# Performance work log

Hardware: AMD Instinct MI355X
Metric: run time of the kernel (lower is better)

The kernel has to match this reference:

```python
import jax, jax.numpy as jnp
import numpy as np

B, V, W, H = 512, 256, 64, 64  # batch, num_variables, window, hidden_size


def setup_inputs() -> dict:
    key = jax.random.key(0)
    ks = jax.random.split(key, 10)
    s = 0.05
    return {
        "x": jax.random.normal(ks[0], (B, V, W), dtype=jnp.float32),
        # nn.LSTM(input=V, hidden=H): gate order i, f, g, o
        "w_ih": jax.random.normal(ks[1], (4 * H, V), dtype=jnp.float32) * s,
        "w_hh": jax.random.normal(ks[2], (4 * H, H), dtype=jnp.float32) * s,
        "b_ih": jax.random.normal(ks[3], (4 * H,), dtype=jnp.float32) * s,
        "b_hh": jax.random.normal(ks[4], (4 * H,), dtype=jnp.float32) * s,
        # linear_v: Linear(window, 1, bias=False)
        "w_v": jax.random.normal(ks[5], (1, W), dtype=jnp.float32) * s,
        # linear_w: Linear(2H, window)
        "w_w": jax.random.normal(ks[6], (W, 2 * H), dtype=jnp.float32) * s,
        "b_w": jax.random.normal(ks[7], (W,), dtype=jnp.float32) * s,
        # linear_u: Linear(window, window)
        "w_u": jax.random.normal(ks[8], (W, W), dtype=jnp.float32) * s,
        "b_u": jax.random.normal(ks[9], (W,), dtype=jnp.float32) * s,
    }


def reference(x, w_ih, w_hh, b_ih, b_hh, w_v, w_w, b_w, w_u, b_u):
    batch, n_var, window = x.shape
    hidden = w_hh.shape[1]
    # linear_u over the window (last) dim: (B, V, W)
    u_out = jnp.einsum("bvw,uw->bvu", x, w_u) + b_u
    x_steps = jnp.transpose(x, (2, 0, 1))  # (W, B, V)

    def step(carry, x_t):
        h, c = carry  # each (B, H)
        # input attention
        wout = jnp.concatenate([h, c], axis=1) @ w_w.T + b_w          # (B, W)
        score = jnp.einsum("bvw,w->bv", jnp.tanh(wout[:, None, :] + u_out), w_v[0])
        alpha = jax.nn.softmax(score, axis=1)                          # (B, V)
        x_tilde = alpha * x_t                                          # (B, V)
        # LSTM cell (torch gate order i, f, g, o)
        gates = x_tilde @ w_ih.T + b_ih + h @ w_hh.T + b_hh            # (B, 4H)
        i_g, f_g, g_g, o_g = jnp.split(gates, 4, axis=1)
        i_g = jax.nn.sigmoid(i_g)
        f_g = jax.nn.sigmoid(f_g)
        g_g = jnp.tanh(g_g)
        o_g = jax.nn.sigmoid(o_g)
        c_new = f_g * c + i_g * g_g
        h_new = o_g * jnp.tanh(c_new)
        return (h_new, c_new), (x_tilde, h_new)

    init = (jnp.zeros((batch, hidden), x.dtype), jnp.zeros((batch, hidden), x.dtype))
    _, (x_tilde_seq, h_seq) = jax.lax.scan(step, init, x_steps)
    # matches torch.stack(x_tilde_list) (W,B,V) and torch.stack(h_list) (W,B,H)
    return x_tilde_seq, h_seq
```

## Files before the change

### kernel.cpp

```cpp
#include <hip/hip_runtime.h>


#define KLOG2E  1.4426950408889634f
#define K2LOG2E 2.8853900817779268f

typedef _Float16 h2    __attribute__((ext_vector_type(2)));
typedef __fp16   f16x8 __attribute__((ext_vector_type(8)));
typedef float    f32x4 __attribute__((ext_vector_type(4)));
union H2U { h2 h; unsigned u; };

__device__ __forceinline__ float frcp(float x)  { return __builtin_amdgcn_rcpf(x); }
__device__ __forceinline__ float fexp2(float x) { return __builtin_amdgcn_exp2f(x); }
__device__ __forceinline__ float fsigmoid(float x) { return frcp(1.f + fexp2(-KLOG2E * x)); }
__device__ __forceinline__ float ftanh(float x) { return 1.f - 2.f * frcp(fexp2(K2LOG2E * x) + 1.f); }

__device__ __forceinline__ unsigned pkrtz_u(float a, float b) {
    H2U r; r.h = __builtin_bit_cast(h2, __builtin_amdgcn_cvt_pkrtz(a, b)); return r.u;
}
__device__ __forceinline__ h2 pk_rtn(float a, float b) {
    h2 r; r.x = (_Float16)a; r.y = (_Float16)b; return r;
}
__device__ __forceinline__ unsigned pk_rtn_u(float a, float b) {
    H2U r; r.h = pk_rtn(a, b); return r.u;
}

#define L_EHA  0
#define L_EHB  9216
#define L_WF   18432
#define L_PSA  34816
#define L_PSB  35072
#define L_XHA  35328
#define L_XHB  35456
#define L_EWA  35584
#define L_EWB  35648
#define L_HCA  35712
#define L_HCB  35840
#define L_HHA  35968
#define L_HHB  36000
#define L_BI   36032
#define L_WV   36288
#define L_WS   36352
#define L_TOT  36368

__global__ __launch_bounds__(1024, 4) void enc_kernel(
    const float* __restrict__ x,
    const float* __restrict__ w_ih,
    const float* __restrict__ w_hh,
    const float* __restrict__ b_ih,
    const float* __restrict__ b_hh,
    const float* __restrict__ w_v,
    const float* __restrict__ w_w,
    const float* __restrict__ b_w,
    const float* __restrict__ w_u,
    const float* __restrict__ b_u,
    float* __restrict__ out_xt,
    float* __restrict__ out_h)
{
    extern __shared__ float lds[];
    unsigned* EHA  = (unsigned*)(lds + L_EHA);
    unsigned* EHB  = (unsigned*)(lds + L_EHB);
    uint4*    WF4  = (uint4*)(lds + L_WF);
    float*    psA  = lds + L_PSA;   float* psB = lds + L_PSB;
    unsigned* xhA  = (unsigned*)(lds + L_XHA);
    unsigned* xhB  = (unsigned*)(lds + L_XHB);
    float*    ewA  = lds + L_EWA;   float* ewB = lds + L_EWB;
    float*    hcA  = lds + L_HCA;   float* hcB = lds + L_HCB;
    unsigned* hhA  = (unsigned*)(lds + L_HHA);
    unsigned* hhB  = (unsigned*)(lds + L_HHB);
    float*    biasL= lds + L_BI;
    float*    wv2L = lds + L_WV;
    float*    wsum = lds + L_WS;

    const int tid  = threadIdx.x;
    const int lane = tid & 63;
    const int wvi  = tid >> 6;
    const int bA   = blockIdx.x;
    const int bB   = blockIdx.x + 256;

    const int colw = wvi*16 + (lane & 15);
    const int kofs = (lane >> 4) * 8;

    const int w8 = wvi*4 + (lane >> 4);
    const int kg = lane & 15;
    const float4 www4 = *(const float4*)&w_w[w8*128 + kg*4];
    const float bwr = b_w[w8];
    float Sv = 0.f;
#pragma unroll
    for (int wi = 0; wi < 64; ++wi) Sv += w_v[wi];
    const float bu_lane = b_u[lane];

    if (tid < 256) biasL[tid] = b_ih[tid] + b_hh[tid];
    if (tid < 64)  wv2L[tid] = -2.f * w_v[tid];
    if (tid < 128) { hcA[tid] = 0.f; hcB[tid] = 0.f; }
    if (tid < 32)  { hhA[tid] = 0u; hhB[tid] = 0u; }

#pragma unroll 1
    for (int bb = 0; bb < 2; ++bb) {
        unsigned* EH = bb ? EHB : EHA;
        const int b = bb ? bB : bA;
        float a0[16];
        {
            float4 wu_r[8];
#pragma unroll
            for (int i = 0; i < 8; ++i) wu_r[i] = *(const float4*)&w_u[lane*64 + 4*i];
            const float* xb = x + b*16384;
#pragma unroll 2
            for (int vi = 0; vi < 16; ++vi) {
                int v = __builtin_amdgcn_readfirstlane(wvi*16 + vi);
                const float4* xr = (const float4*)(xb + v*64);
                float acc = 0.f;
#pragma unroll
                for (int i = 0; i < 8; ++i) {
                    float4 xx = xr[i]; float4 wu = wu_r[i];
                    acc += xx.x*wu.x + xx.y*wu.y + xx.z*wu.z + xx.w*wu.w;
                }
                a0[vi] = acc;
            }
        }
        {
            float4 wu_r[8];
#pragma unroll
            for (int i = 0; i < 8; ++i) wu_r[i] = *(const float4*)&w_u[lane*64 + 32 + 4*i];
            const float* xb = x + b*16384 + 32;
#pragma unroll 2
            for (int vi = 0; vi < 16; ++vi) {
                int v = __builtin_amdgcn_readfirstlane(wvi*16 + vi);
                const float4* xr = (const float4*)(xb + v*64);
                float acc = a0[vi] + bu_lane;
#pragma unroll
                for (int i = 0; i < 8; ++i) {
                    float4 xx = xr[i]; float4 wu = wu_r[i];
                    acc += xx.x*wu.x + xx.y*wu.y + xx.z*wu.z + xx.w*wu.w;
                }
                float e = fexp2(K2LOG2E * acc);
                float e2 = __shfl_xor(e, 1, 64);
                if (!(lane & 1)) EH[v*36 + (lane >> 1)] = pk_rtn_u(e, e2);
            }
        }
    }

    f16x8 wbx[4], wbh[2];
#pragma unroll
    for (int kk = 0; kk < 4; ++kk) {
        const float* s = w_ih + colw*256 + kk*32 + kofs;
        f16x8 a;
#pragma unroll
        for (int i = 0; i < 8; ++i) a[i] = (__fp16)s[i];
        wbx[kk] = a;
    }
#pragma unroll
    for (int kk = 0; kk < 2; ++kk) {
        const float* s = w_hh + colw*64 + kk*32 + kofs;
        f16x8 a;
#pragma unroll
        for (int i = 0; i < 8; ++i) a[i] = (__fp16)s[i];
        wbh[kk] = a;
    }
#pragma unroll
    for (int kk = 4; kk < 8; ++kk) {
        const float* s = w_ih + colw*256 + kk*32 + kofs;
        uint4 u;
        u.x = pk_rtn_u(s[0], s[1]);
        u.y = pk_rtn_u(s[2], s[3]);
        u.z = pk_rtn_u(s[4], s[5]);
        u.w = pk_rtn_u(s[6], s[7]);
        WF4[(wvi*4 + (kk - 4))*64 + lane] = u;
    }
    __syncthreads();

    const int xj   = (tid & 511) >> 1;
    const int hf   = tid & 1;
    const int bsel = tid >> 9;
    const uint4* EHrow4 = (const uint4*)((bsel ? EHB : EHA) + xj*36 + hf*16);
    const float* ewS = (bsel ? ewB : ewA) + hf*32;
    const float* wvS = wv2L + hf*32;
    unsigned*    xhX = bsel ? xhB : xhA;
    const float  SvIni = hf ? 0.f : Sv;
    const float* xrow = x + (bsel ? bB : bA)*16384 + xj*64;
    float xcur = hf ? 0.f : xrow[0];

    const int mrow = lane & 15;
    const int q4   = (lane >> 4) * 4;

    for (int t = 0; t < 64; ++t) {
        {
            float4 hA = *(const float4*)&hcA[kg*4];
            float4 hB = *(const float4*)&hcB[kg*4];
            float accA = hA.x*www4.x + hA.y*www4.y + hA.z*www4.z + hA.w*www4.w;
            float accB = hB.x*www4.x + hB.y*www4.y + hB.z*www4.z + hB.w*www4.w;
#pragma unroll
            for (int off = 1; off <= 8; off <<= 1) {
                accA += __shfl_xor(accA, off, 64);
                accB += __shfl_xor(accB, off, 64);
            }
            if (kg == 0)      ewA[w8] = fexp2(K2LOG2E * (accA + bwr));
            else if (kg == 1) ewB[w8] = fexp2(K2LOG2E * (accB + bwr));
        }
        float xnxt = (hf == 0 && t < 63) ? xrow[t + 1] : 0.f;
        __syncthreads();

        float exreg;
        {
            float ac0 = SvIni, ac1 = 0.f, ac2 = 0.f, ac3 = 0.f;
#pragma unroll
            for (int i = 0; i < 4; ++i) {
                uint4 U = EHrow4[i];
                float4 c0 = *(const float4*)&ewS[8*i];
                float4 c1 = *(const float4*)&ewS[8*i + 4];
                float4 v0 = *(const float4*)&wvS[8*i];
                float4 v1 = *(const float4*)&wvS[8*i + 4];
                H2U u0, u1, u2, u3;
                u0.u = U.x; u1.u = U.y; u2.u = U.z; u3.u = U.w;
                ac0 += v0.x * frcp((float)u0.h.x * c0.x + 1.f);
                ac1 += v0.y * frcp((float)u0.h.y * c0.y + 1.f);
                ac2 += v0.z * frcp((float)u1.h.x * c0.z + 1.f);
                ac3 += v0.w * frcp((float)u1.h.y * c0.w + 1.f);
                ac0 += v1.x * frcp((float)u2.h.x * c1.x + 1.f);
                ac1 += v1.y * frcp((float)u2.h.y * c1.y + 1.f);
                ac2 += v1.z * frcp((float)u3.h.x * c1.z + 1.f);
                ac3 += v1.w * frcp((float)u3.h.y * c1.w + 1.f);
            }
            float acc = (ac0 + ac1) + (ac2 + ac3);
            acc += __shfl_xor(acc, 1, 64);
            float e = fexp2(KLOG2E * acc);
            exreg = e * xcur;
            float s = e;
            s += __shfl_xor(s, 2, 64);  s += __shfl_xor(s, 4, 64);
            s += __shfl_xor(s, 8, 64);  s += __shfl_xor(s, 16, 64);
            s += __shfl_xor(s, 32, 64);
            if (lane == 0) wsum[wvi] = s;
            float exhi = __shfl_xor(exreg, 2, 64);
            if ((lane & 3) == 0) xhX[xj >> 1] = pkrtz_u(exreg, exhi);
        }
        xcur = xnxt;
        __syncthreads();

        {
            float rA = frcp(((wsum[0] + wsum[1]) + (wsum[2] + wsum[3]))
                          + ((wsum[4] + wsum[5]) + (wsum[6] + wsum[7])));
            float rB = frcp(((wsum[8] + wsum[9]) + (wsum[10] + wsum[11]))
                          + ((wsum[12] + wsum[13]) + (wsum[14] + wsum[15])));
            if (hf == 0)
                out_xt[t*131072 + (bsel ? bB : bA)*256 + xj] = (bsel ? rB : rA) * exreg;

            f32x4 ax = {0.f,0.f,0.f,0.f}, ah = {0.f,0.f,0.f,0.f};
            const unsigned* xsrc = (mrow == 1) ? xhB : xhA;
#pragma unroll
            for (int kk = 0; kk < 8; ++kk) {
                f16x8 a = {};
                if (mrow < 2)
                    a = __builtin_bit_cast(f16x8, *(const uint4*)(xsrc + kk*16 + q4));
                f16x8 bf;
                if (kk < 4) bf = wbx[kk];
                else        bf = __builtin_bit_cast(f16x8, WF4[(wvi*4 + (kk - 4))*64 + lane]);
                ax = __builtin_amdgcn_mfma_f32_16x16x32_f16(a, bf, ax, 0, 0, 0);
            }
            const unsigned* hsrc = (mrow == 1) ? hhB : hhA;
#pragma unroll
            for (int kk = 0; kk < 2; ++kk) {
                f16x8 a = {};
                if (mrow < 2)
                    a = __builtin_bit_cast(f16x8, *(const uint4*)(hsrc + kk*16 + q4));
                ah = __builtin_amdgcn_mfma_f32_16x16x32_f16(a, wbh[kk], ah, 0, 0, 0);
            }
            if (lane < 16) {
                psA[wvi*16 + lane] = rA*ax[0] + ah[0];
                psB[wvi*16 + lane] = rB*ax[1] + ah[1];
            }
        }
        __syncthreads();

        if (wvi < 2) {
            float*    ps = wvi ? psB : psA;
            float*    hc = wvi ? hcB : hcA;
            unsigned* hh = wvi ? hhB : hhA;
            float*    oh = out_h + t*32768 + (wvi ? bB : bA)*64;
            const int k = lane;
            float gi = fsigmoid(biasL[k      ] + ps[k      ]);
            float gf = fsigmoid(biasL[64  + k] + ps[64  + k]);
            float gg = ftanh   (biasL[128 + k] + ps[128 + k]);
            float go = fsigmoid(biasL[192 + k] + ps[192 + k]);
            float cn = gf * hc[64 + k] + gi * gg;
            float hn = go * ftanh(cn);
            hc[k] = hn; hc[64 + k] = cn;
            float hp = __shfl_xor(hn, 1, 64);
            if (!(lane & 1)) hh[k >> 1] = pkrtz_u(hn, hp);
            oh[k] = hn;
        }
        __syncthreads();
    }
}

extern "C" void kernel_launch(void* const* d_in, const int* in_sizes, int n_in,
                              void* d_out, int out_size, void* d_ws, size_t ws_size,
                              hipStream_t stream) {
    const float* x    = (const float*)d_in[0];
    const float* w_ih = (const float*)d_in[1];
    const float* w_hh = (const float*)d_in[2];
    const float* b_ih = (const float*)d_in[3];
    const float* b_hh = (const float*)d_in[4];
    const float* w_v  = (const float*)d_in[5];
    const float* w_w  = (const float*)d_in[6];
    const float* b_w  = (const float*)d_in[7];
    const float* w_u  = (const float*)d_in[8];
    const float* b_u  = (const float*)d_in[9];

    float* out_xt = (float*)d_out;
    float* out_h  = out_xt + 64*512*256;

    const size_t shbytes = (size_t)L_TOT * sizeof(float);
    (void)hipFuncSetAttribute((const void*)enc_kernel,
                        hipFuncAttributeMaxDynamicSharedMemorySize, (int)shbytes);
    enc_kernel<<<dim3(256), dim3(1024), shbytes, stream>>>(
        x, w_ih, w_hh, b_ih, b_hh, w_v, w_w, b_w, w_u, b_u, out_xt, out_h);
}
```

Before: 275.4 us.

## Fuse LSTM cell update into gate MFMA waves and drop a per-step barrier

Rows of w_ih and w_hh are permuted so that each wave's 16 MFMA output columns hold the i, f, g and o gates for four hidden cells. The cell update then runs in registers through lane shuffles, with the cell state kept per lane. This removes the gate-sum LDS buffer, the bias LDS table and one __syncthreads per timestep. The recurrent h MFMA is moved earlier so it can overlap the attention stage. The attention projection now also includes the c half of w_w, which the earlier code left out. That fixes correctness but adds a little work each step.

```diff
diff --git a/kernel.cpp b/kernel.cpp
--- a/kernel.cpp
+++ b/kernel.cpp
@@ -27,20 +27,17 @@
 #define L_EHA  0
 #define L_EHB  9216
 #define L_WF   18432
-#define L_PSA  34816
-#define L_PSB  35072
-#define L_XHA  35328
-#define L_XHB  35456
-#define L_EWA  35584
-#define L_EWB  35648
-#define L_HCA  35712
-#define L_HCB  35840
-#define L_HHA  35968
-#define L_HHB  36000
-#define L_BI   36032
-#define L_WV   36288
-#define L_WS   36352
-#define L_TOT  36368
+#define L_XHA  34816
+#define L_XHB  34944
+#define L_EWA  35072
+#define L_EWB  35136
+#define L_HCA  35200
+#define L_HCB  35328
+#define L_HHA  35456
+#define L_HHB  35488
+#define L_WV   35520
+#define L_WS   35584
+#define L_TOT  35600
 
 __global__ __launch_bounds__(1024, 4) void enc_kernel(
     const float* __restrict__ x,
@@ -60,14 +57,12 @@
     unsigned* EHA  = (unsigned*)(lds + L_EHA);
     unsigned* EHB  = (unsigned*)(lds + L_EHB);
     uint4*    WF4  = (uint4*)(lds + L_WF);
-    float*    psA  = lds + L_PSA;   float* psB = lds + L_PSB;
     unsigned* xhA  = (unsigned*)(lds + L_XHA);
     unsigned* xhB  = (unsigned*)(lds + L_XHB);
     float*    ewA  = lds + L_EWA;   float* ewB = lds + L_EWB;
     float*    hcA  = lds + L_HCA;   float* hcB = lds + L_HCB;
     unsigned* hhA  = (unsigned*)(lds + L_HHA);
     unsigned* hhB  = (unsigned*)(lds + L_HHB);
-    float*    biasL= lds + L_BI;
     float*    wv2L = lds + L_WV;
     float*    wsum = lds + L_WS;
 
@@ -77,19 +72,23 @@
     const int bA   = blockIdx.x;
     const int bB   = blockIdx.x + 256;
 
-    const int colw = wvi*16 + (lane & 15);
+    const int qg   = lane & 3;
+    const int mc   = (lane & 15) >> 2;
+    const int kcell= wvi*4 + mc;
+    const int rowp = qg*64 + kcell;
     const int kofs = (lane >> 4) * 8;
 
     const int w8 = wvi*4 + (lane >> 4);
     const int kg = lane & 15;
-    const float4 www4 = *(const float4*)&w_w[w8*128 + kg*4];
+    const float4 wwa = *(const float4*)&w_w[w8*128 + kg*4];
+    const float4 wwb = *(const float4*)&w_w[w8*128 + 64 + kg*4];
     const float bwr = b_w[w8];
     float Sv = 0.f;
 #pragma unroll
     for (int wi = 0; wi < 64; ++wi) Sv += w_v[wi];
     const float bu_lane = b_u[lane];
-
-    if (tid < 256) biasL[tid] = b_ih[tid] + b_hh[tid];
+    const float bias_r = b_ih[rowp] + b_hh[rowp];
+
     if (tid < 64)  wv2L[tid] = -2.f * w_v[tid];
     if (tid < 128) { hcA[tid] = 0.f; hcB[tid] = 0.f; }
     if (tid < 32)  { hhA[tid] = 0u; hhB[tid] = 0u; }
@@ -142,7 +141,7 @@
     f16x8 wbx[4], wbh[2];
 #pragma unroll
     for (int kk = 0; kk < 4; ++kk) {
-        const float* s = w_ih + colw*256 + kk*32 + kofs;
+        const float* s = w_ih + rowp*256 + kk*32 + kofs;
         f16x8 a;
 #pragma unroll
         for (int i = 0; i < 8; ++i) a[i] = (__fp16)s[i];
@@ -150,7 +149,7 @@
     }
 #pragma unroll
     for (int kk = 0; kk < 2; ++kk) {
-        const float* s = w_hh + colw*64 + kk*32 + kofs;
+        const float* s = w_hh + rowp*64 + kk*32 + kofs;
         f16x8 a;
 #pragma unroll
         for (int i = 0; i < 8; ++i) a[i] = (__fp16)s[i];
@@ -158,7 +157,7 @@
     }
 #pragma unroll
     for (int kk = 4; kk < 8; ++kk) {
-        const float* s = w_ih + colw*256 + kk*32 + kofs;
+        const float* s = w_ih + rowp*256 + kk*32 + kofs;
         uint4 u;
         u.x = pk_rtn_u(s[0], s[1]);
         u.y = pk_rtn_u(s[2], s[3]);
@@ -182,12 +181,27 @@
     const int mrow = lane & 15;
     const int q4   = (lane >> 4) * 4;
 
+    float cregA = 0.f, cregB = 0.f;
+
     for (int t = 0; t < 64; ++t) {
+        f32x4 ah = {0.f,0.f,0.f,0.f};
         {
             float4 hA = *(const float4*)&hcA[kg*4];
+            float4 cA = *(const float4*)&hcA[64 + kg*4];
             float4 hB = *(const float4*)&hcB[kg*4];
-            float accA = hA.x*www4.x + hA.y*www4.y + hA.z*www4.z + hA.w*www4.w;
-            float accB = hB.x*www4.x + hB.y*www4.y + hB.z*www4.z + hB.w*www4.w;
+            float4 cB = *(const float4*)&hcB[64 + kg*4];
+            float accA = (hA.x*wwa.x + hA.y*wwa.y + hA.z*wwa.z + hA.w*wwa.w)
+                       + (cA.x*wwb.x + cA.y*wwb.y + cA.z*wwb.z + cA.w*wwb.w);
+            float accB = (hB.x*wwa.x + hB.y*wwa.y + hB.z*wwa.z + hB.w*wwa.w)
+                       + (cB.x*wwb.x + cB.y*wwb.y + cB.z*wwb.z + cB.w*wwb.w);
+            const unsigned* hsrc = (mrow == 1) ? hhB : hhA;
+#pragma unroll
+            for (int kk = 0; kk < 2; ++kk) {
+                f16x8 a = {};
+                if (mrow < 2)
+                    a = __builtin_bit_cast(f16x8, *(const uint4*)(hsrc + kk*16 + q4));
+                ah = __builtin_amdgcn_mfma_f32_16x16x32_f16(a, wbh[kk], ah, 0, 0, 0);
+            }
 #pragma unroll
             for (int off = 1; off <= 8; off <<= 1) {
                 accA += __shfl_xor(accA, off, 64);
@@ -243,7 +257,7 @@
             if (hf == 0)
                 out_xt[t*131072 + (bsel ? bB : bA)*256 + xj] = (bsel ? rB : rA) * exreg;
 
-            f32x4 ax = {0.f,0.f,0.f,0.f}, ah = {0.f,0.f,0.f,0.f};
+            f32x4 ax = {0.f,0.f,0.f,0.f};
             const unsigned* xsrc = (mrow == 1) ? xhB : xhA;
 #pragma unroll
             for (int kk = 0; kk < 8; ++kk) {
@@ -255,37 +269,31 @@
                 else        bf = __builtin_bit_cast(f16x8, WF4[(wvi*4 + (kk - 4))*64 + lane]);
                 ax = __builtin_amdgcn_mfma_f32_16x16x32_f16(a, bf, ax, 0, 0, 0);
             }
-            const unsigned* hsrc = (mrow == 1) ? hhB : hhA;
-#pragma unroll
-            for (int kk = 0; kk < 2; ++kk) {
-                f16x8 a = {};
-                if (mrow < 2)
-                    a = __builtin_bit_cast(f16x8, *(const uint4*)(hsrc + kk*16 + q4));
-                ah = __builtin_amdgcn_mfma_f32_16x16x32_f16(a, wbh[kk], ah, 0, 0, 0);
-            }
-            if (lane < 16) {
-                psA[wvi*16 + lane] = rA*ax[0] + ah[0];
-                psB[wvi*16 + lane] = rB*ax[1] + ah[1];
-            }
-        }
-        __syncthreads();
-
-        if (wvi < 2) {
-            float*    ps = wvi ? psB : psA;
-            float*    hc = wvi ? hcB : hcA;
-            unsigned* hh = wvi ? hhB : hhA;
-            float*    oh = out_h + t*32768 + (wvi ? bB : bA)*64;
-            const int k = lane;
-            float gi = fsigmoid(biasL[k      ] + ps[k      ]);
-            float gf = fsigmoid(biasL[64  + k] + ps[64  + k]);
-            float gg = ftanh   (biasL[128 + k] + ps[128 + k]);
-            float go = fsigmoid(biasL[192 + k] + ps[192 + k]);
-            float cn = gf * hc[64 + k] + gi * gg;
-            float hn = go * ftanh(cn);
-            hc[k] = hn; hc[64 + k] = cn;
-            float hp = __shfl_xor(hn, 1, 64);
-            if (!(lane & 1)) hh[k >> 1] = pkrtz_u(hn, hp);
-            oh[k] = hn;
+            float gA = rA*ax[0] + ah[0] + bias_r;
+            float gB = rB*ax[1] + ah[1] + bias_r;
+            const int base = lane & ~3;
+            float giA = __shfl(gA, base    , 64), giB = __shfl(gB, base    , 64);
+            float gfA = __shfl(gA, base | 1, 64), gfB = __shfl(gB, base | 1, 64);
+            float ggA = __shfl(gA, base | 2, 64), ggB = __shfl(gB, base | 2, 64);
+            float goA = __shfl(gA, base | 3, 64), goB = __shfl(gB, base | 3, 64);
+            giA = fsigmoid(giA); gfA = fsigmoid(gfA); ggA = ftanh(ggA); goA = fsigmoid(goA);
+            giB = fsigmoid(giB); gfB = fsigmoid(gfB); ggB = ftanh(ggB); goB = fsigmoid(goB);
+            cregA = gfA*cregA + giA*ggA;
+            cregB = gfB*cregB + giB*ggB;
+            float hnA = goA * ftanh(cregA);
+            float hnB = goB * ftanh(cregB);
+            float hpA = __shfl(hnA, (lane + 4) & 63, 64);
+            float hpB = __shfl(hnB, (lane + 4) & 63, 64);
+            if (lane < 16 && qg == 0) {
+                hcA[kcell] = hnA; hcA[64 + kcell] = cregA;
+                hcB[kcell] = hnB; hcB[64 + kcell] = cregB;
+                out_h[t*32768 + bA*64 + kcell] = hnA;
+                out_h[t*32768 + bB*64 + kcell] = hnB;
+                if ((mc & 1) == 0) {
+                    hhA[kcell >> 1] = pkrtz_u(hnA, hpA);
+                    hhB[kcell >> 1] = pkrtz_u(hnB, hpB);
+                }
+            }
         }
         __syncthreads();
     }
```

Result: slower. 295.3 us (+7.3%).
